# Kernel optimization log

Measured on AMD Instinct MI355X. Metric: run time of the kernel, lower is better.

The kernel has to match this reference:

```python
import jax, jax.numpy as jnp
import numpy as np

D_MODEL, D_K, D_V, HEAD = 512, 512, 512, 8
SCALE = 1.0 / np.sqrt(D_K)  # torch code divides by sqrt(d_k) (full d_k, not head_dim)
NEG = -1.0e9


def setup_inputs() -> dict:
    key = jax.random.key(0)
    ks = jax.random.split(key, 10)
    B, S = 2, 4096
    x = jax.random.normal(ks[0], (B, S, D_MODEL), dtype=jnp.float32)
    mask = jax.random.randint(ks[1], (B, S), 0, 2, dtype=jnp.int32)
    s = 1.0 / np.sqrt(D_MODEL)
    Wq = jax.random.normal(ks[2], (D_MODEL, D_K), dtype=jnp.float32) * s
    bq = jnp.zeros((D_K,), jnp.float32)
    Wk = jax.random.normal(ks[3], (D_MODEL, D_K), dtype=jnp.float32) * s
    bk = jnp.zeros((D_K,), jnp.float32)
    Wv = jax.random.normal(ks[4], (D_MODEL, D_V), dtype=jnp.float32) * s
    bv = jnp.zeros((D_V,), jnp.float32)
    Wo = jax.random.normal(ks[5], (D_V, D_MODEL), dtype=jnp.float32) * s
    bo = jnp.zeros((D_MODEL,), jnp.float32)
    return {"x": x, "mask": mask, "Wq": Wq, "bq": bq, "Wk": Wk, "bk": bk,
            "Wv": Wv, "bv": bv, "Wo": Wo, "bo": bo}


def reference(x, mask, Wq, bq, Wk, bk, Wv, bv, Wo, bo):
    B, S, _ = x.shape
    hd_k = D_K // HEAD
    hd_v = D_V // HEAD
    # projections -> [B, H, S, hd]
    Q = (x @ Wq + bq).reshape(B, S, HEAD, hd_k).transpose(0, 2, 1, 3)
    K = (x @ Wk + bk).reshape(B, S, HEAD, hd_k).transpose(0, 2, 1, 3)
    V = (x @ Wv + bv).reshape(B, S, HEAD, hd_v).transpose(0, 2, 1, 3)
    # scores [B, H, S, S], scaled by 1/sqrt(d_k) (full d_k, faithful to source)
    scores = jnp.einsum('bhqd,bhkd->bhqk', Q, K) * SCALE
    m = (mask == 1)[:, None, None, :]  # [B,1,1,S]
    scores = jnp.where(m, NEG, scores)
    attn = jax.nn.softmax(scores, axis=-1)
    out = jnp.einsum('bhqk,bhkd->bhqd', attn, V)  # [B,H,S,hd_v]
    out = out.transpose(0, 2, 1, 3).reshape(B, S, D_V)
    return out @ Wo + bo
```

## Files before the change

kernel.cpp:

```cpp
#include <hip/hip_runtime.h>
#include <hip/hip_bf16.h>
#include <stdint.h>

typedef __attribute__((ext_vector_type(8))) short bf16x8;
typedef __attribute__((ext_vector_type(4))) float f32x4;
typedef __attribute__((ext_vector_type(16))) float f32x16;
typedef __attribute__((ext_vector_type(4))) unsigned int u32x4;

#define MFMA16(a, b, c) __builtin_amdgcn_mfma_f32_16x16x32_bf16(a, b, c, 0, 0, 0)
#define MFMA32(a, b, c) __builtin_amdgcn_mfma_f32_32x32x16_bf16(a, b, c, 0, 0, 0)

constexpr float QSCALE = 0.04419417382415922f * 1.4426950408889634f;

__device__ __forceinline__ void gload_lds16(const void* g, void* l) {
  __builtin_amdgcn_global_load_lds((const __attribute__((address_space(1))) uint32_t*)g,
                                   (__attribute__((address_space(3))) uint32_t*)l, 16, 0, 0);
}
__device__ __forceinline__ bf16x8 lds_read_swz(const short* base, int row, int ch) {
  return *(const bf16x8*)((const char*)base + row * 128 + (((ch ^ row) & 7) << 4));
}
__device__ __forceinline__ short f2b(float f) {
  __hip_bfloat16 h = __float2bfloat16(f);
  return *reinterpret_cast<short*>(&h);
}
__device__ __forceinline__ float exp2fast(float x) {
#if __has_builtin(__builtin_amdgcn_exp2f)
  return __builtin_amdgcn_exp2f(x);
#else
  return exp2f(x);
#endif
}

__global__ void k_cvt_x(const float* __restrict__ x, short* __restrict__ xb) {
  const int i = blockIdx.x * 256 + threadIdx.x;
  const float4 v = ((const float4*)x)[i];
  short4 o;
  o.x = f2b(v.x); o.y = f2b(v.y); o.z = f2b(v.z); o.w = f2b(v.w);
  ((short4*)xb)[i] = o;
}

__global__ void k_cvt_w(const float* __restrict__ wq, const float* __restrict__ wk,
                        const float* __restrict__ wv, const float* __restrict__ wo,
                        short* __restrict__ wt) {
  const int gid = blockIdx.x * 256 + threadIdx.x;
  const int mat = gid >> 18;
  const int idx = gid & 262143;
  const int n = idx >> 9, k = idx & 511;
  const float* w = (mat == 0) ? wq : (mat == 1) ? wk : (mat == 2) ? wv : wo;
  wt[gid] = f2b(w[k * 512 + n]);
}

__global__ void k_scan(const int* __restrict__ mask, int* __restrict__ perm,
                       int* __restrict__ cnt) {
  __shared__ int ws[16];
  const int b = blockIdx.x, tid = threadIdx.x;
  const int lane = tid & 63, w = tid >> 6;
  const int* m = mask + b * 4096;
  int v[4], s = 0;
#pragma unroll
  for (int j = 0; j < 4; ++j) { v[j] = (m[tid * 4 + j] == 0) ? 1 : 0; s += v[j]; }
  int sc = s;
  for (int d = 1; d < 64; d <<= 1) { int t = __shfl_up(sc, d); if (lane >= d) sc += t; }
  if (lane == 63) ws[w] = sc;
  __syncthreads();
  if (tid == 0) {
    int acc = 0;
    for (int i = 0; i < 16; ++i) { int t = ws[i]; ws[i] = acc; acc += t; }
    cnt[b] = acc;
  }
  __syncthreads();
  int pos = ws[w] + sc - s;
  int* p = perm + b * 4096;
#pragma unroll
  for (int j = 0; j < 4; ++j) { p[tid * 4 + j] = v[j] ? pos : -1; pos += v[j]; }
}

template <int MODE>
__global__ __launch_bounds__(256, 2) void k_gemm(
    const short* __restrict__ A, const short* __restrict__ W,
    const float* __restrict__ bias0, const float* __restrict__ bias1,
    const float* __restrict__ bias2, const int* __restrict__ perm,
    short* __restrict__ oq, short* __restrict__ ok, short* __restrict__ ov,
    float* __restrict__ fo) {
  __shared__ short Asm[2][128 * 64];
  __shared__ short Bsm[2][64 * 64];
  const int tid = threadIdx.x;
  const int wave = tid >> 6, lane = tid & 63;
  const int lane15 = lane & 15, g = lane >> 4;
  const int wm = wave >> 1, wn = wave & 1;
  const int m0 = blockIdx.x * 128;

  int mat = 0, n0, h = 0;
  const float* bptr;
  if constexpr (MODE == 0) {
    mat = blockIdx.y >> 3; h = blockIdx.y & 7; n0 = h * 64;
    bptr = (mat == 0) ? bias0 : (mat == 1) ? bias1 : bias2;
  } else {
    n0 = blockIdx.y * 64; bptr = bias0;
  }
  const char* Ag = (const char*)A + (size_t)m0 * 1024;
  const char* Bg = (const char*)(W + (size_t)mat * (512 * 512)) + (size_t)n0 * 1024;

  f32x4 acc[4][2] = {};

  auto stage = [&](int buf, int kt) {
    const int k0b = kt * 128;
#pragma unroll
    for (int q = 0; q < 4; ++q) {
      int s_ = (wave * 4 + q) * 64 + lane;
      int row = s_ >> 3, ch = s_ & 7;
      gload_lds16(Ag + (size_t)row * 1024 + k0b + (((ch ^ row) & 7) << 4),
                  (char*)&Asm[buf][0] + s_ * 16);
    }
#pragma unroll
    for (int q = 0; q < 2; ++q) {
      int s_ = (wave * 2 + q) * 64 + lane;
      int row = s_ >> 3, ch = s_ & 7;
      gload_lds16(Bg + (size_t)row * 1024 + k0b + (((ch ^ row) & 7) << 4),
                  (char*)&Bsm[buf][0] + s_ * 16);
    }
  };

  stage(0, 0);
  asm volatile("s_waitcnt vmcnt(0)" ::: "memory");
  __syncthreads();

  for (int kt = 0; kt < 8; ++kt) {
    const int cur = kt & 1;
    if (kt < 7) stage(cur ^ 1, kt + 1);
#pragma unroll
    for (int kk = 0; kk < 2; ++kk) {
      bf16x8 af[4], bfr[2];
#pragma unroll
      for (int m = 0; m < 4; ++m)
        af[m] = lds_read_swz(&Asm[cur][0], wm * 64 + m * 16 + lane15, kk * 4 + g);
#pragma unroll
      for (int n = 0; n < 2; ++n)
        bfr[n] = lds_read_swz(&Bsm[cur][0], wn * 32 + n * 16 + lane15, kk * 4 + g);
#pragma unroll
      for (int m = 0; m < 4; ++m)
#pragma unroll
        for (int n = 0; n < 2; ++n)
          acc[m][n] = MFMA16(af[m], bfr[n], acc[m][n]);
    }
    asm volatile("s_waitcnt vmcnt(0)" ::: "memory");
    __syncthreads();
  }

#pragma unroll
  for (int n = 0; n < 2; ++n) {
    const int d = wn * 32 + n * 16 + lane15;
    const float bias = bptr[n0 + d];
#pragma unroll
    for (int m = 0; m < 4; ++m) {
#pragma unroll
      for (int j = 0; j < 4; ++j) {
        const int rowg = m0 + wm * 64 + m * 16 + g * 4 + j;
        float v = acc[m][n][j] + bias;
        if constexpr (MODE == 0) {
          const int b_ = rowg >> 12, sl = rowg & 4095;
          const size_t bh = (size_t)(b_ * 8 + h);
          if (mat == 0) {
            const int qt32 = sl >> 5, l31q = sl & 31;
            const int dk = d >> 4, hb = (d >> 3) & 1, jj = d & 7;
            oq[bh * 262144 + (size_t)((qt32 * 4 + dk) * 64 + hb * 32 + l31q) * 8 + jj] =
                f2b(v * QSCALE);
          } else {
            const int pm = perm[b_ * 4096 + sl];
            if (pm >= 0) {
              const int t = pm >> 6, r = pm & 63;
              if (mat == 1) {
                const int x = r >> 5, l31k = r & 31;
                const int dk = d >> 4, hb = (d >> 3) & 1, jj = d & 7;
                ok[bh * 262144 + (size_t)((t * 8 + dk * 2 + x) * 64 + hb * 32 + l31k) * 8 + jj] =
                    f2b(v);
              } else {
                const int mm = (r & ~12) | (((r >> 2) & 1) << 3) | (((r >> 3) & 1) << 2);
                const int s = (mm >> 4) & 3, hb = (mm >> 3) & 1, jj = mm & 7;
                const int x = d >> 5, l31v = d & 31;
                ov[bh * 262144 + (size_t)((t * 8 + s * 2 + x) * 64 + hb * 32 + l31v) * 8 + jj] =
                    f2b(v);
              }
            }
          }
        } else {
          fo[(size_t)rowg * 512 + n0 + d] = v;
        }
      }
    }
  }
}

#define ATT_BODY(T, KC, KN)                                                   \
  {                                                                           \
    bf16x8 v0_ = vld(T, 0), v1_ = vld(T, 1), v2_ = vld(T, 2), v3_ = vld(T, 3),\
           v4_ = vld(T, 4), v5_ = vld(T, 5), v6_ = vld(T, 6), v7_ = vld(T, 7);\
    f32x16 s0v = {}, s1v = {};                                                \
    __builtin_amdgcn_s_setprio(1);                                            \
    _Pragma("unroll") for (int dk = 0; dk < 4; ++dk) {                        \
      s0v = MFMA32(KC[2 * dk], qreg[dk], s0v);                                \
      s1v = MFMA32(KC[2 * dk + 1], qreg[dk], s1v);                            \
    }                                                                         \
    __builtin_amdgcn_s_setprio(0);                                            \
    _Pragma("unroll") for (int u = 0; u < 8; ++u) KN[u] = kld((T) + 1, u);    \
    if ((T) == nt - 1 && lim < 64) {                                          \
      _Pragma("unroll") for (int i = 0; i < 16; ++i) {                        \
        const int r0 = (i & 3) + 8 * (i >> 2) + 4 * h;                        \
        if (r0 >= lim) s0v[i] = -1e30f;                                       \
        if (r0 + 32 >= lim) s1v[i] = -1e30f;                                  \
      }                                                                       \
    }                                                                         \
    float pm = s0v[0];                                                        \
    _Pragma("unroll") for (int i = 1; i < 16; ++i) pm = fmaxf(pm, s0v[i]);    \
    _Pragma("unroll") for (int i = 0; i < 16; ++i) pm = fmaxf(pm, s1v[i]);    \
    pm = fmaxf(pm, __shfl_xor(pm, 32));                                       \
    if (__any(pm > m_ + 8.f)) {                                               \
      const float nm = fmaxf(m_, pm);                                         \
      const float sc = exp2fast(m_ - nm);                                     \
      m_ = nm; l_ *= sc; o0 = o0 * sc; o1 = o1 * sc;                          \
    }                                                                         \
    unsigned int wA[8], wB[8];                                                \
    float ts = 0.f;                                                           \
    _Pragma("unroll") for (int j2 = 0; j2 < 8; ++j2) {                        \
      float a0 = exp2fast(s0v[2 * j2] - m_);                                  \
      float a1 = exp2fast(s0v[2 * j2 + 1] - m_);                              \
      float b0 = exp2fast(s1v[2 * j2] - m_);                                  \
      float b1 = exp2fast(s1v[2 * j2 + 1] - m_);                              \
      ts += (a0 + a1) + (b0 + b1);                                            \
      asm("v_cvt_pk_bf16_f32 %0, %1, %2" : "=v"(wA[j2]) : "v"(a0), "v"(a1));  \
      asm("v_cvt_pk_bf16_f32 %0, %1, %2" : "=v"(wB[j2]) : "v"(b0), "v"(b1));  \
    }                                                                         \
    ts += __shfl_xor(ts, 32);                                                 \
    l_ += ts;                                                                 \
    __builtin_amdgcn_s_setprio(1);                                            \
    {                                                                         \
      union PU { u32x4 u; bf16x8 f; } pu;                                     \
      pu.u[0] = wA[0]; pu.u[1] = wA[1]; pu.u[2] = wA[2]; pu.u[3] = wA[3];     \
      o0 = MFMA32(v0_, pu.f, o0); o1 = MFMA32(v1_, pu.f, o1);                 \
      pu.u[0] = wA[4]; pu.u[1] = wA[5]; pu.u[2] = wA[6]; pu.u[3] = wA[7];     \
      o0 = MFMA32(v2_, pu.f, o0); o1 = MFMA32(v3_, pu.f, o1);                 \
      pu.u[0] = wB[0]; pu.u[1] = wB[1]; pu.u[2] = wB[2]; pu.u[3] = wB[3];     \
      o0 = MFMA32(v4_, pu.f, o0); o1 = MFMA32(v5_, pu.f, o1);                 \
      pu.u[0] = wB[4]; pu.u[1] = wB[5]; pu.u[2] = wB[6]; pu.u[3] = wB[7];     \
      o0 = MFMA32(v6_, pu.f, o0); o1 = MFMA32(v7_, pu.f, o1);                 \
    }                                                                         \
    __builtin_amdgcn_s_setprio(0);                                            \
  }

__global__ __launch_bounds__(256, 2) void k_attn(
    const short* __restrict__ Qp, const short* __restrict__ Kp,
    const short* __restrict__ Vp, const int* __restrict__ cnt,
    short* __restrict__ out) {
  const int tid = threadIdx.x;
  const int wave = tid >> 6, lane = tid & 63;
  const int l31 = lane & 31, h = lane >> 5;
  const int bh = blockIdx.y, b = bh >> 3, hh = bh & 7;
  const int qb = blockIdx.x * 4 + wave;

  const short* Qg = Qp + (size_t)bh * 262144;
  const short* Kg = Kp + (size_t)bh * 262144;
  const short* Vg = Vp + (size_t)bh * 262144;

  auto kld = [&](int t, int u) {
    return *(const bf16x8*)(Kg + ((size_t)(t * 8 + u) * 64 + lane) * 8);
  };
  auto vld = [&](int t, int u) {
    return *(const bf16x8*)(Vg + ((size_t)(t * 8 + u) * 64 + lane) * 8);
  };

  bf16x8 qreg[4];
#pragma unroll
  for (int dk = 0; dk < 4; ++dk)
    qreg[dk] = *(const bf16x8*)(Qg + ((size_t)(qb * 4 + dk) * 64 + lane) * 8);

  const int cn = cnt[b];
  const int nt = max(1, (cn + 63) >> 6);
  const int lim = cn - (nt - 1) * 64;

  bf16x8 ka[8], kb[8];
#pragma unroll
  for (int u = 0; u < 8; ++u) ka[u] = kld(0, u);

  f32x16 o0 = {}, o1 = {};
  float m_ = -1.0e30f, l_ = 0.f;

  for (int t = 0; t < nt; t += 2) {
    ATT_BODY(t, ka, kb);
    if (t + 1 < nt) ATT_BODY(t + 1, kb, ka);
  }

  const float inv = 1.0f / l_;
  short* og = out + (size_t)(b * 4096 + qb * 32 + l31) * 512 + hh * 64;
#pragma unroll
  for (int r2 = 0; r2 < 4; ++r2) {
    {
      const int base = 8 * r2 + 4 * h;
      short4 s4;
      s4.x = f2b(o0[4 * r2 + 0] * inv);
      s4.y = f2b(o0[4 * r2 + 1] * inv);
      s4.z = f2b(o0[4 * r2 + 2] * inv);
      s4.w = f2b(o0[4 * r2 + 3] * inv);
      *(short4*)(og + base) = s4;
    }
    {
      const int base = 32 + 8 * r2 + 4 * h;
      short4 s4;
      s4.x = f2b(o1[4 * r2 + 0] * inv);
      s4.y = f2b(o1[4 * r2 + 1] * inv);
      s4.z = f2b(o1[4 * r2 + 2] * inv);
      s4.w = f2b(o1[4 * r2 + 3] * inv);
      *(short4*)(og + base) = s4;
    }
  }
}

extern "C" void kernel_launch(void* const* d_in, const int* in_sizes, int n_in,
                              void* d_out, int out_size, void* d_ws, size_t ws_size,
                              hipStream_t stream) {
  const float* x  = (const float*)d_in[0];
  const int* mask = (const int*)d_in[1];
  const float* Wq = (const float*)d_in[2];
  const float* bq = (const float*)d_in[3];
  const float* Wk = (const float*)d_in[4];
  const float* bk = (const float*)d_in[5];
  const float* Wv = (const float*)d_in[6];
  const float* bv = (const float*)d_in[7];
  const float* Wo = (const float*)d_in[8];
  const float* bo = (const float*)d_in[9];
  float* out = (float*)d_out;

  short* xb   = (short*)d_ws;
  short* wt   = xb + (size_t)8192 * 512;
  short* qws  = wt + (size_t)4 * 512 * 512;
  short* kws  = qws + (size_t)8192 * 512;
  short* vws  = kws + (size_t)8192 * 512;
  short* aout = vws + (size_t)8192 * 512;
  int* perm   = (int*)(aout + (size_t)8192 * 512);
  int* cntw   = perm + 8192;

  k_cvt_x<<<4096, 256, 0, stream>>>(x, xb);
  k_cvt_w<<<4096, 256, 0, stream>>>(Wq, Wk, Wv, Wo, wt);
  k_scan<<<2, 1024, 0, stream>>>(mask, perm, cntw);
  k_gemm<0><<<dim3(64, 24), 256, 0, stream>>>(xb, wt, bq, bk, bv, perm, qws, kws, vws, nullptr);
  k_attn<<<dim3(32, 16), 256, 0, stream>>>(qws, kws, vws, cntw, aout);
  k_gemm<1><<<dim3(64, 8), 256, 0, stream>>>(aout, wt + (size_t)3 * 512 * 512, bo, nullptr,
                                             nullptr, nullptr, nullptr, nullptr, nullptr, out);
}
```

Before: 193.6 us.

## Split attention over KV halves with combine kernel; enlarge GEMM tiles to 128x128

The attention kernel gains a second grid dimension that splits the key tiles into two halves. Each half writes unnormalized fp32 partial outputs plus its running max and sum to workspace, and a new combine kernel merges them into the bf16 attention output. The split doubles the number of attention blocks, raising occupancy on a device where 512 blocks underfill the CUs. Separately, the GEMMs move to 128x128 tiles with a 4x4 MFMA accumulator per wave and s_setprio around the MFMA loop, halving the block count. The cost is extra fp32 partial traffic and one more kernel launch.

```diff
diff --git a/kernel.cpp b/kernel.cpp
--- a/kernel.cpp
+++ b/kernel.cpp
@@ -76,32 +76,25 @@
 }
 
 template <int MODE>
-__global__ __launch_bounds__(256, 2) void k_gemm(
+__global__ __launch_bounds__(256, 2) void k_gemm2(
     const short* __restrict__ A, const short* __restrict__ W,
-    const float* __restrict__ bias0, const float* __restrict__ bias1,
-    const float* __restrict__ bias2, const int* __restrict__ perm,
+    const float* __restrict__ bq, const float* __restrict__ bk,
+    const float* __restrict__ bv, const int* __restrict__ perm,
     short* __restrict__ oq, short* __restrict__ ok, short* __restrict__ ov,
     float* __restrict__ fo) {
   __shared__ short Asm[2][128 * 64];
-  __shared__ short Bsm[2][64 * 64];
+  __shared__ short Bsm[2][128 * 64];
   const int tid = threadIdx.x;
   const int wave = tid >> 6, lane = tid & 63;
   const int lane15 = lane & 15, g = lane >> 4;
   const int wm = wave >> 1, wn = wave & 1;
   const int m0 = blockIdx.x * 128;
-
-  int mat = 0, n0, h = 0;
-  const float* bptr;
-  if constexpr (MODE == 0) {
-    mat = blockIdx.y >> 3; h = blockIdx.y & 7; n0 = h * 64;
-    bptr = (mat == 0) ? bias0 : (mat == 1) ? bias1 : bias2;
-  } else {
-    n0 = blockIdx.y * 64; bptr = bias0;
-  }
+  const int n0 = blockIdx.y * 128;
+
   const char* Ag = (const char*)A + (size_t)m0 * 1024;
-  const char* Bg = (const char*)(W + (size_t)mat * (512 * 512)) + (size_t)n0 * 1024;
-
-  f32x4 acc[4][2] = {};
+  const char* Bg = (const char*)W + (size_t)n0 * 1024;
+
+  f32x4 acc[4][4] = {};
 
   auto stage = [&](int buf, int kt) {
     const int k0b = kt * 128;
@@ -111,11 +104,6 @@
       int row = s_ >> 3, ch = s_ & 7;
       gload_lds16(Ag + (size_t)row * 1024 + k0b + (((ch ^ row) & 7) << 4),
                   (char*)&Asm[buf][0] + s_ * 16);
-    }
-#pragma unroll
-    for (int q = 0; q < 2; ++q) {
-      int s_ = (wave * 2 + q) * 64 + lane;
-      int row = s_ >> 3, ch = s_ & 7;
       gload_lds16(Bg + (size_t)row * 1024 + k0b + (((ch ^ row) & 7) << 4),
                   (char*)&Bsm[buf][0] + s_ * 16);
     }
@@ -130,63 +118,72 @@
     if (kt < 7) stage(cur ^ 1, kt + 1);
 #pragma unroll
     for (int kk = 0; kk < 2; ++kk) {
-      bf16x8 af[4], bfr[2];
+      bf16x8 af[4], bfr[4];
 #pragma unroll
       for (int m = 0; m < 4; ++m)
         af[m] = lds_read_swz(&Asm[cur][0], wm * 64 + m * 16 + lane15, kk * 4 + g);
 #pragma unroll
-      for (int n = 0; n < 2; ++n)
-        bfr[n] = lds_read_swz(&Bsm[cur][0], wn * 32 + n * 16 + lane15, kk * 4 + g);
+      for (int n = 0; n < 4; ++n)
+        bfr[n] = lds_read_swz(&Bsm[cur][0], wn * 64 + n * 16 + lane15, kk * 4 + g);
+      __builtin_amdgcn_s_setprio(1);
 #pragma unroll
       for (int m = 0; m < 4; ++m)
 #pragma unroll
-        for (int n = 0; n < 2; ++n)
+        for (int n = 0; n < 4; ++n)
           acc[m][n] = MFMA16(af[m], bfr[n], acc[m][n]);
+      __builtin_amdgcn_s_setprio(0);
     }
     asm volatile("s_waitcnt vmcnt(0)" ::: "memory");
     __syncthreads();
   }
 
 #pragma unroll
-  for (int n = 0; n < 2; ++n) {
-    const int d = wn * 32 + n * 16 + lane15;
-    const float bias = bptr[n0 + d];
-#pragma unroll
-    for (int m = 0; m < 4; ++m) {
-#pragma unroll
-      for (int j = 0; j < 4; ++j) {
-        const int rowg = m0 + wm * 64 + m * 16 + g * 4 + j;
-        float v = acc[m][n][j] + bias;
-        if constexpr (MODE == 0) {
+  for (int nf = 0; nf < 4; ++nf) {
+    const int col = n0 + wn * 64 + nf * 16 + lane15;
+    if constexpr (MODE == 0) {
+      const int mat = col >> 9, nn = col & 511;
+      const int hh = nn >> 6, d = nn & 63;
+      const float bias = ((mat == 0) ? bq : (mat == 1) ? bk : bv)[nn];
+      const int dk = d >> 4, hb = (d >> 3) & 1, jj = d & 7;
+#pragma unroll
+      for (int mf = 0; mf < 4; ++mf) {
+#pragma unroll
+        for (int j = 0; j < 4; ++j) {
+          const int rowg = m0 + wm * 64 + mf * 16 + g * 4 + j;
           const int b_ = rowg >> 12, sl = rowg & 4095;
-          const size_t bh = (size_t)(b_ * 8 + h);
+          const size_t bh = (size_t)(b_ * 8 + hh);
+          const float v = acc[mf][nf][j] + bias;
           if (mat == 0) {
-            const int qt32 = sl >> 5, l31q = sl & 31;
-            const int dk = d >> 4, hb = (d >> 3) & 1, jj = d & 7;
-            oq[bh * 262144 + (size_t)((qt32 * 4 + dk) * 64 + hb * 32 + l31q) * 8 + jj] =
+            oq[bh * 262144 +
+               (size_t)(((sl >> 5) * 4 + dk) * 64 + hb * 32 + (sl & 31)) * 8 + jj] =
                 f2b(v * QSCALE);
           } else {
-            const int pm = perm[b_ * 4096 + sl];
-            if (pm >= 0) {
-              const int t = pm >> 6, r = pm & 63;
+            const int pm_ = perm[b_ * 4096 + sl];
+            if (pm_ >= 0) {
+              const int t = pm_ >> 6, r = pm_ & 63;
               if (mat == 1) {
-                const int x = r >> 5, l31k = r & 31;
-                const int dk = d >> 4, hb = (d >> 3) & 1, jj = d & 7;
-                ok[bh * 262144 + (size_t)((t * 8 + dk * 2 + x) * 64 + hb * 32 + l31k) * 8 + jj] =
+                ok[bh * 262144 +
+                   (size_t)((t * 8 + dk * 2 + (r >> 5)) * 64 + hb * 32 + (r & 31)) * 8 + jj] =
                     f2b(v);
               } else {
                 const int mm = (r & ~12) | (((r >> 2) & 1) << 3) | (((r >> 3) & 1) << 2);
-                const int s = (mm >> 4) & 3, hb = (mm >> 3) & 1, jj = mm & 7;
-                const int x = d >> 5, l31v = d & 31;
-                ov[bh * 262144 + (size_t)((t * 8 + s * 2 + x) * 64 + hb * 32 + l31v) * 8 + jj] =
-                    f2b(v);
+                ov[bh * 262144 +
+                   (size_t)((t * 8 + ((mm >> 4) & 3) * 2 + (d >> 5)) * 64 +
+                            ((mm >> 3) & 1) * 32 + (d & 31)) * 8 + (mm & 7)] = f2b(v);
               }
             }
           }
-        } else {
-          fo[(size_t)rowg * 512 + n0 + d] = v;
         }
       }
+    } else {
+      const float bias = bq[col];
+#pragma unroll
+      for (int mf = 0; mf < 4; ++mf)
+#pragma unroll
+        for (int j = 0; j < 4; ++j) {
+          const int rowg = m0 + wm * 64 + mf * 16 + g * 4 + j;
+          fo[(size_t)rowg * 512 + col] = acc[mf][nf][j] + bias;
+        }
     }
   }
 }
@@ -250,6 +247,65 @@
 __global__ __launch_bounds__(256, 2) void k_attn(
     const short* __restrict__ Qp, const short* __restrict__ Kp,
     const short* __restrict__ Vp, const int* __restrict__ cnt,
+    float* __restrict__ Op, float* __restrict__ Ml) {
+  const int tid = threadIdx.x;
+  const int wave = tid >> 6, lane = tid & 63;
+  const int l31 = lane & 31, h = lane >> 5;
+  const int bh = blockIdx.y, b = bh >> 3;
+  const int z = blockIdx.z;
+  const int qb = blockIdx.x * 4 + wave;
+
+  const short* Qg = Qp + (size_t)bh * 262144;
+  const short* Kg = Kp + (size_t)bh * 262144;
+  const short* Vg = Vp + (size_t)bh * 262144;
+
+  auto kld = [&](int t, int u) {
+    return *(const bf16x8*)(Kg + ((size_t)(t * 8 + u) * 64 + lane) * 8);
+  };
+  auto vld = [&](int t, int u) {
+    return *(const bf16x8*)(Vg + ((size_t)(t * 8 + u) * 64 + lane) * 8);
+  };
+
+  bf16x8 qreg[4];
+#pragma unroll
+  for (int dk = 0; dk < 4; ++dk)
+    qreg[dk] = *(const bf16x8*)(Qg + ((size_t)(qb * 4 + dk) * 64 + lane) * 8);
+
+  const int cn = cnt[b];
+  const int nt = max(1, (cn + 63) >> 6);
+  const int lim = cn - (nt - 1) * 64;
+  const int half = (nt + 1) >> 1;
+  const int t0 = z ? half : 0;
+  const int t1 = z ? nt : half;
+
+  bf16x8 ka[8], kb[8];
+  f32x16 o0 = {}, o1 = {};
+  float m_ = -1.0e30f, l_ = 0.f;
+
+  if (t0 < t1) {
+#pragma unroll
+    for (int u = 0; u < 8; ++u) ka[u] = kld(t0, u);
+    for (int t = t0; t < t1; t += 2) {
+      ATT_BODY(t, ka, kb);
+      if (t + 1 < t1) ATT_BODY(t + 1, kb, ka);
+    }
+  }
+
+  float* ob = Op + ((size_t)(z * 16 + bh) * 128 + qb) * 2048 + lane * 32;
+  union OU { f32x16 v; float f[16]; } u0, u1;
+  u0.v = o0; u1.v = o1;
+#pragma unroll
+  for (int i = 0; i < 16; ++i) ob[i] = u0.f[i];
+#pragma unroll
+  for (int i = 0; i < 16; ++i) ob[16 + i] = u1.f[i];
+  if (h == 0) {
+    float2 ml; ml.x = m_; ml.y = l_;
+    ((float2*)Ml)[((size_t)(z * 16 + bh) * 128 + qb) * 32 + l31] = ml;
+  }
+}
+
+__global__ __launch_bounds__(256, 4) void k_comb(
+    const float* __restrict__ Op, const float* __restrict__ Ml,
     short* __restrict__ out) {
   const int tid = threadIdx.x;
   const int wave = tid >> 6, lane = tid & 63;
@@ -257,58 +313,45 @@
   const int bh = blockIdx.y, b = bh >> 3, hh = bh & 7;
   const int qb = blockIdx.x * 4 + wave;
 
-  const short* Qg = Qp + (size_t)bh * 262144;
-  const short* Kg = Kp + (size_t)bh * 262144;
-  const short* Vg = Vp + (size_t)bh * 262144;
-
-  auto kld = [&](int t, int u) {
-    return *(const bf16x8*)(Kg + ((size_t)(t * 8 + u) * 64 + lane) * 8);
-  };
-  auto vld = [&](int t, int u) {
-    return *(const bf16x8*)(Vg + ((size_t)(t * 8 + u) * 64 + lane) * 8);
-  };
-
-  bf16x8 qreg[4];
-#pragma unroll
-  for (int dk = 0; dk < 4; ++dk)
-    qreg[dk] = *(const bf16x8*)(Qg + ((size_t)(qb * 4 + dk) * 64 + lane) * 8);
-
-  const int cn = cnt[b];
-  const int nt = max(1, (cn + 63) >> 6);
-  const int lim = cn - (nt - 1) * 64;
-
-  bf16x8 ka[8], kb[8];
-#pragma unroll
-  for (int u = 0; u < 8; ++u) ka[u] = kld(0, u);
-
-  f32x16 o0 = {}, o1 = {};
-  float m_ = -1.0e30f, l_ = 0.f;
-
-  for (int t = 0; t < nt; t += 2) {
-    ATT_BODY(t, ka, kb);
-    if (t + 1 < nt) ATT_BODY(t + 1, kb, ka);
-  }
-
-  const float inv = 1.0f / l_;
+  const float2 ml0 = ((const float2*)Ml)[((size_t)(0 * 16 + bh) * 128 + qb) * 32 + l31];
+  const float2 ml1 = ((const float2*)Ml)[((size_t)(1 * 16 + bh) * 128 + qb) * 32 + l31];
+  const float nm = fmaxf(ml0.x, ml1.x);
+  const float w0 = exp2fast(ml0.x - nm), w1 = exp2fast(ml1.x - nm);
+  const float inv = 1.0f / (w0 * ml0.y + w1 * ml1.y);
+  const float a0 = w0 * inv, a1 = w1 * inv;
+
+  const float* p0 = Op + ((size_t)(0 * 16 + bh) * 128 + qb) * 2048 + lane * 32;
+  const float* p1 = Op + ((size_t)(1 * 16 + bh) * 128 + qb) * 2048 + lane * 32;
+  float r[32];
+#pragma unroll
+  for (int i = 0; i < 8; ++i) {
+    const float4 x0 = ((const float4*)p0)[i];
+    const float4 x1 = ((const float4*)p1)[i];
+    r[4 * i + 0] = x0.x * a0 + x1.x * a1;
+    r[4 * i + 1] = x0.y * a0 + x1.y * a1;
+    r[4 * i + 2] = x0.z * a0 + x1.z * a1;
+    r[4 * i + 3] = x0.w * a0 + x1.w * a1;
+  }
+
   short* og = out + (size_t)(b * 4096 + qb * 32 + l31) * 512 + hh * 64;
 #pragma unroll
   for (int r2 = 0; r2 < 4; ++r2) {
     {
       const int base = 8 * r2 + 4 * h;
       short4 s4;
-      s4.x = f2b(o0[4 * r2 + 0] * inv);
-      s4.y = f2b(o0[4 * r2 + 1] * inv);
-      s4.z = f2b(o0[4 * r2 + 2] * inv);
-      s4.w = f2b(o0[4 * r2 + 3] * inv);
+      s4.x = f2b(r[4 * r2 + 0]);
+      s4.y = f2b(r[4 * r2 + 1]);
+      s4.z = f2b(r[4 * r2 + 2]);
+      s4.w = f2b(r[4 * r2 + 3]);
       *(short4*)(og + base) = s4;
     }
     {
       const int base = 32 + 8 * r2 + 4 * h;
       short4 s4;
-      s4.x = f2b(o1[4 * r2 + 0] * inv);
-      s4.y = f2b(o1[4 * r2 + 1] * inv);
-      s4.z = f2b(o1[4 * r2 + 2] * inv);
-      s4.w = f2b(o1[4 * r2 + 3] * inv);
+      s4.x = f2b(r[16 + 4 * r2 + 0]);
+      s4.y = f2b(r[16 + 4 * r2 + 1]);
+      s4.z = f2b(r[16 + 4 * r2 + 2]);
+      s4.w = f2b(r[16 + 4 * r2 + 3]);
       *(short4*)(og + base) = s4;
     }
   }
@@ -335,14 +378,19 @@
   short* kws  = qws + (size_t)8192 * 512;
   short* vws  = kws + (size_t)8192 * 512;
   short* aout = vws + (size_t)8192 * 512;
-  int* perm   = (int*)(aout + (size_t)8192 * 512);
+  float* opart = (float*)(aout + (size_t)8192 * 512);
+  float* mlp   = opart + (size_t)2 * 16 * 128 * 2048;
+  int* perm   = (int*)(mlp + (size_t)2 * 16 * 128 * 32 * 2);
   int* cntw   = perm + 8192;
 
   k_cvt_x<<<4096, 256, 0, stream>>>(x, xb);
   k_cvt_w<<<4096, 256, 0, stream>>>(Wq, Wk, Wv, Wo, wt);
   k_scan<<<2, 1024, 0, stream>>>(mask, perm, cntw);
-  k_gemm<0><<<dim3(64, 24), 256, 0, stream>>>(xb, wt, bq, bk, bv, perm, qws, kws, vws, nullptr);
-  k_attn<<<dim3(32, 16), 256, 0, stream>>>(qws, kws, vws, cntw, aout);
-  k_gemm<1><<<dim3(64, 8), 256, 0, stream>>>(aout, wt + (size_t)3 * 512 * 512, bo, nullptr,
-                                             nullptr, nullptr, nullptr, nullptr, nullptr, out);
-}
+  k_gemm2<0><<<dim3(64, 12), 256, 0, stream>>>(xb, wt, bq, bk, bv, perm,
+                                               qws, kws, vws, nullptr);
+  k_attn<<<dim3(32, 16, 2), 256, 0, stream>>>(qws, kws, vws, cntw, opart, mlp);
+  k_comb<<<dim3(32, 16), 256, 0, stream>>>(opart, mlp, aout);
+  k_gemm2<1><<<dim3(64, 4), 256, 0, stream>>>(aout, wt + (size_t)3 * 512 * 512, bo,
+                                              nullptr, nullptr, nullptr,
+                                              nullptr, nullptr, nullptr, out);
+}
```

Result: slower. 209.6 us (+8.3%).
